# Optimization experiments

Hardware: AMD Instinct MI355X
Metric: run time of the kernel (lower is better)

Reference implementation:

```python
import jax, jax.numpy as jnp
import numpy as np

N, E, CIN, H, OUT, L = 100000, 1200000, 3, 64, 3, 3
EPS = 1e-7  # GENConv message epsilon


def setup_inputs() -> dict:
    key = jax.random.key(0)
    ks = jax.random.split(key, 8)
    f = lambda k, s, sc=0.1: (jax.random.normal(k, s, jnp.float32) * sc)
    return {
        "x": f(ks[0], (N, CIN), 1.0),
        "edge_index": jax.random.randint(ks[1], (2, E), 0, N, jnp.int32),
        "enc_W": f(ks[2], (CIN, H)),
        "enc_b": jnp.zeros((H,), jnp.float32),
        "t": jnp.ones((L,), jnp.float32),
        "mlp_W1": f(ks[3], (L, H, 2 * H)),
        "mlp_b1": jnp.zeros((L, 2 * H), jnp.float32),
        "mlp_g": jnp.ones((L, 2 * H), jnp.float32),
        "mlp_beta": jnp.zeros((L, 2 * H), jnp.float32),
        "mlp_W2": f(ks[4], (L, 2 * H, H)),
        "mlp_b2": jnp.zeros((L, H), jnp.float32),
        "ln_g": jnp.ones((L, H), jnp.float32),
        "ln_b": jnp.zeros((L, H), jnp.float32),
        "lin_W": f(ks[5], (H, OUT)),
        "lin_b": jnp.zeros((OUT,), jnp.float32),
    }


def layer_norm(x, g, b, eps=1e-5):
    mu = jnp.mean(x, -1, keepdims=True)
    var = jnp.var(x, -1, keepdims=True)
    return (x - mu) * jax.lax.rsqrt(var + eps) * g + b


def genconv(x, src, dst, t, W1, b1, g, beta, W2, b2):
    # message: relu(x_j) + eps, per edge  [E, H]
    msg = jax.nn.relu(x[src]) + EPS
    # softmax aggregation with temperature t (per-destination, elementwise)
    logits = msg * t
    m = jax.ops.segment_max(logits, dst, num_segments=N)            # [N, H]
    w = jnp.exp(logits - m[dst])                                    # [E, H]
    denom = jax.ops.segment_sum(w, dst, num_segments=N)             # [N, H]
    agg = jax.ops.segment_sum(msg * (w / denom[dst]), dst, num_segments=N)
    # root residual + MLP [H -> 2H -> LN -> ReLU -> H]
    out = agg + x
    h = jax.nn.relu(layer_norm(out @ W1 + b1, g, beta))
    return h @ W2 + b2


def reference(x, edge_index, enc_W, enc_b, t, mlp_W1, mlp_b1, mlp_g, mlp_beta,
              mlp_W2, mlp_b2, ln_g, ln_b, lin_W, lin_b):
    src, dst = edge_index[0], edge_index[1]
    h = x @ enc_W + enc_b
    # layers[0].conv applied directly (DeepGCN 'res+' convention)
    h = genconv(h, src, dst, t[0], mlp_W1[0], mlp_b1[0], mlp_g[0], mlp_beta[0],
                mlp_W2[0], mlp_b2[0])
    for i in range(1, L):
        z = jax.nn.relu(layer_norm(h, ln_g[i], ln_b[i]))
        h = h + genconv(z, src, dst, t[i], mlp_W1[i], mlp_b1[i], mlp_g[i],
                        mlp_beta[i], mlp_W2[i], mlp_b2[i])
    h = jax.nn.relu(layer_norm(h, ln_g[0], ln_b[0]))
    return h @ lin_W + lin_b
```

## Files before the change

### kernel.cpp

```cpp
#include <hip/hip_runtime.h>
#include <hip/hip_bf16.h>
#include <math.h>

#define H 64
#define H2 128
#define EPS_MSG 1e-7f
#define LN_EPS 1e-5f
#define LOG2E 1.4426950408889634f
#define LN2 0.6931471805599453f
#define YSTR 136
#define BSTRIDE 4608
#define OSTRIDE 5376
#define CHUNK 8192

typedef __attribute__((ext_vector_type(8))) short bf16x8;
typedef __attribute__((ext_vector_type(4))) float f32x4;

__device__ __forceinline__ unsigned short f2bf(float f) {
    union { float f; unsigned int i; } x; x.f = f;
    unsigned int r = x.i + 0x7FFF + ((x.i >> 16) & 1);
    return (unsigned short)(r >> 16);
}

__global__ __launch_bounds__(256) void bscat_k(const int* __restrict__ src,
                                               const int* __restrict__ dst,
                                               int* __restrict__ bcnt,
                                               unsigned int* __restrict__ bdata,
                                               int E, int nbuck) {
    __shared__ int h[512], base[512];
    for (int i = threadIdx.x; i < nbuck; i += 256) h[i] = 0;
    __syncthreads();
    int lo = blockIdx.x * CHUNK;
    int hi = lo + CHUNK; if (hi > E) hi = E;
    for (int i = lo + threadIdx.x; i < hi; i += 256)
        atomicAdd(&h[dst[i] >> 8], 1);
    __syncthreads();
    for (int i = threadIdx.x; i < nbuck; i += 256) {
        int c = h[i];
        base[i] = c ? atomicAdd(&bcnt[i], c) : 0;
        h[i] = 0;
    }
    __syncthreads();
    for (int i = lo + threadIdx.x; i < hi; i += 256) {
        int d = dst[i];
        int b = d >> 8;
        int pos = base[b] + atomicAdd(&h[b], 1);
        bdata[(size_t)b * BSTRIDE + pos] = ((unsigned int)src[i] << 8) | (unsigned int)(d & 255);
    }
}

__global__ __launch_bounds__(256) void bsort_k(const unsigned int* __restrict__ bdata,
                                               const int* __restrict__ bcnt,
                                               int2* __restrict__ rowq,
                                               int* __restrict__ srcs_sorted,
                                               int Nn) {
    __shared__ unsigned int stage[BSTRIDE];
    __shared__ int cnt[256], pre[256], ex[256];
    int b = blockIdx.x, tid = threadIdx.x;
    int m = bcnt[b]; if (m > BSTRIDE) m = BSTRIDE;
    size_t lo = (size_t)b * BSTRIDE;
    int oLo = b * OSTRIDE;
    for (int i = tid; i < m; i += 256) stage[i] = bdata[lo + i];
    cnt[tid] = 0;
    __syncthreads();
    for (int i = tid; i < m; i += 256) atomicAdd(&cnt[stage[i] & 255], 1);
    __syncthreads();
    int myc = cnt[tid];
    int pc = (myc + 3) & ~3;
    pre[tid] = pc;
    __syncthreads();
    #pragma unroll
    for (int off = 1; off < 256; off <<= 1) {
        int t = (tid >= off) ? pre[tid - off] : 0;
        __syncthreads();
        pre[tid] += t;
        __syncthreads();
    }
    int pexcl = pre[tid] - pc;
    ex[tid] = pexcl;
    int node = (b << 8) + tid;
    if (node < Nn) rowq[node] = make_int2(oLo + pexcl, pc >> 2);
    else           rowq[node] = make_int2(0, 0);
    for (int p = myc; p < pc; ++p) srcs_sorted[oLo + pexcl + p] = Nn;
    __syncthreads();
    cnt[tid] = 0;
    __syncthreads();
    for (int i = tid; i < m; i += 256) {
        unsigned int v = stage[i];
        int dl = v & 255;
        int p = ex[dl] + atomicAdd(&cnt[dl], 1);
        srcs_sorted[oLo + p] = (int)(v >> 8);
    }
}

__global__ void wprep_k(const float* __restrict__ W1, const float* __restrict__ W2,
                        unsigned short* __restrict__ Wf1, unsigned short* __restrict__ Wf2) {
    int idx = blockIdx.x * 256 + threadIdx.x;
    const int half = 3 * 8192;
    if (idx < half) {
        int layer = idx / 8192, rem = idx - layer * 8192;
        int t = rem >> 9;
        int l = (rem >> 3) & 63;
        int i = rem & 7;
        int h = t >> 3, ct = t & 7;
        int kpos = h * 32 + (l >> 4) * 8 + i;
        int k = (kpos & 3) * 16 + (kpos >> 2);
        int j = ct * 16 + (l & 15);
        Wf1[idx] = f2bf(W1[(size_t)layer * H * H2 + (size_t)k * H2 + j]);
    } else if (idx < 2 * half) {
        int id2 = idx - half;
        int layer = id2 / 8192, rem = id2 - layer * 8192;
        int t = rem >> 9;
        int l = (rem >> 3) & 63;
        int i = rem & 7;
        int kk = t >> 2, ct2 = t & 3;
        int k = kk * 32 + (l >> 4) * 8 + i;
        int j = ct2 * 16 + (l & 15);
        Wf2[id2] = f2bf(W2[(size_t)layer * H2 * H + (size_t)k * H + j]);
    }
}

__global__ void encoder_k(const float* __restrict__ x, const float* __restrict__ W,
                          const float* __restrict__ b,
                          unsigned short* __restrict__ Zself, unsigned short* __restrict__ Zmsg,
                          const float* __restrict__ t, int Nn) {
    int idx = blockIdx.x * blockDim.x + threadIdx.x;
    if (idx >= (Nn + 1) * H) return;
    int n = idx >> 6, c = idx & 63;
    if (n == Nn) { Zmsg[idx] = f2bf(-200.f); return; }
    float acc = b[c];
    #pragma unroll
    for (int k = 0; k < 3; ++k) acc = fmaf(x[n * 3 + k], W[k * H + c], acc);
    int j = (c & 15) * 4 + (c >> 4);
    Zself[(size_t)n * H + j] = f2bf(acc);
    Zmsg[(size_t)n * H + j]  = f2bf(fmaxf(acc, 0.f) * (LOG2E) * t[0]);
}

__global__ __launch_bounds__(256) void gather_k(
    const unsigned short* __restrict__ Zmsg, const unsigned short* __restrict__ Zself,
    unsigned short* __restrict__ Gbf,
    const int2* __restrict__ rowq,
    const int* __restrict__ srcs,
    const float* __restrict__ t, int layer, int Nn)
{
    int wid = threadIdx.x >> 6, lane = threadIdx.x & 63;
    int nA = (blockIdx.x * 4 + wid) * 4;
    if (nA >= Nn) return;
    int slot = lane >> 4;
    int ch4  = lane & 15;
    float scale = (LN2) * __builtin_amdgcn_rcpf(t[layer]);

    int4 rAB = *(const int4*)&rowq[nA];
    int4 rCD = *(const int4*)&rowq[nA + 2];
    int begA = rAB.x, qA = rAB.y, begB = rAB.z, qB = rAB.w;
    int begC = rCD.x, qC = rCD.y, begD = rCD.z, qD = rCD.w;

    int ns = nA + slot; if (ns >= Nn) ns = Nn - 1;
    const unsigned short* selfTab = (layer == 0) ? Zself : Zmsg;
    uint2 sv = *(const uint2*)(selfTab + (size_t)ns * H + ch4 * 4);

    #define LQ(qq, beg, i)                                                     \
        {                                                                      \
            int s = srcs[(beg) + 4 * (i) + slot];                              \
            qq = *(const uint2*)(Zmsg + (size_t)s * H + ch4 * 4);              \
        }

    uint2 a0={0,0},a1={0,0},a2={0,0},a3={0,0};
    uint2 b0={0,0},b1={0,0},b2={0,0},b3={0,0};
    uint2 c0={0,0},c1={0,0},c2={0,0},c3={0,0};
    uint2 e0={0,0},e1={0,0},e2={0,0},e3={0,0};
    if (qA > 0) LQ(a0, begA, 0)
    if (qB > 0) LQ(b0, begB, 0)
    if (qC > 0) LQ(c0, begC, 0)
    if (qD > 0) LQ(e0, begD, 0)
    if (qA > 1) LQ(a1, begA, 1)
    if (qB > 1) LQ(b1, begB, 1)
    if (qC > 1) LQ(c1, begC, 1)
    if (qD > 1) LQ(e1, begD, 1)
    if (qA > 2) LQ(a2, begA, 2)
    if (qB > 2) LQ(b2, begB, 2)
    if (qC > 2) LQ(c2, begC, 2)
    if (qD > 2) LQ(e2, begD, 2)
    if (qA > 3) LQ(a3, begA, 3)
    if (qB > 3) LQ(b3, begB, 3)
    if (qC > 3) LQ(c3, begC, 3)
    if (qD > 3) LQ(e3, begD, 3)

    float dA0=0.f,dA1=0.f,dA2=0.f,dA3=0.f,sA0=0.f,sA1=0.f,sA2=0.f,sA3=0.f;
    float dB0=0.f,dB1=0.f,dB2=0.f,dB3=0.f,sB0=0.f,sB1=0.f,sB2=0.f,sB3=0.f;
    float dC0=0.f,dC1=0.f,dC2=0.f,dC3=0.f,sC0=0.f,sC1=0.f,sC2=0.f,sC3=0.f;
    float dD0=0.f,dD1=0.f,dD2=0.f,dD3=0.f,sD0=0.f,sD1=0.f,sD2=0.f,sD3=0.f;

    #define PROC(qq, dd0,dd1,dd2,dd3, ss0,ss1,ss2,ss3)                         \
        {                                                                      \
            float u0 = __uint_as_float(qq.x << 16);                            \
            float u1 = __uint_as_float(qq.x & 0xffff0000u);                    \
            float u2 = __uint_as_float(qq.y << 16);                            \
            float u3 = __uint_as_float(qq.y & 0xffff0000u);                    \
            float w0 = __builtin_amdgcn_exp2f(u0);                             \
            float w1 = __builtin_amdgcn_exp2f(u1);                             \
            float w2 = __builtin_amdgcn_exp2f(u2);                             \
            float w3 = __builtin_amdgcn_exp2f(u3);                             \
            dd0 += w0; dd1 += w1; dd2 += w2; dd3 += w3;                        \
            ss0 = fmaf(u0, w0, ss0); ss1 = fmaf(u1, w1, ss1);                  \
            ss2 = fmaf(u2, w2, ss2); ss3 = fmaf(u3, w3, ss3);                  \
        }
    #define PROCA(qq) PROC(qq, dA0,dA1,dA2,dA3, sA0,sA1,sA2,sA3)
    #define PROCB(qq) PROC(qq, dB0,dB1,dB2,dB3, sB0,sB1,sB2,sB3)
    #define PROCC(qq) PROC(qq, dC0,dC1,dC2,dC3, sC0,sC1,sC2,sC3)
    #define PROCD(qq) PROC(qq, dD0,dD1,dD2,dD3, sD0,sD1,sD2,sD3)

    if (qA > 0) {
        int i = 0;
        #pragma unroll 1
        for (; i + 4 < qA; i += 4) {
            PROCA(a0) LQ(a0, begA, i + 4)
            PROCA(a1) if (i + 5 < qA) LQ(a1, begA, i + 5)
            PROCA(a2) if (i + 6 < qA) LQ(a2, begA, i + 6)
            PROCA(a3) if (i + 7 < qA) LQ(a3, begA, i + 7)
        }
        PROCA(a0)
        if (i + 1 < qA) PROCA(a1)
        if (i + 2 < qA) PROCA(a2)
        if (i + 3 < qA) PROCA(a3)
    }
    if (qB > 0) {
        int i = 0;
        #pragma unroll 1
        for (; i + 4 < qB; i += 4) {
            PROCB(b0) LQ(b0, begB, i + 4)
            PROCB(b1) if (i + 5 < qB) LQ(b1, begB, i + 5)
            PROCB(b2) if (i + 6 < qB) LQ(b2, begB, i + 6)
            PROCB(b3) if (i + 7 < qB) LQ(b3, begB, i + 7)
        }
        PROCB(b0)
        if (i + 1 < qB) PROCB(b1)
        if (i + 2 < qB) PROCB(b2)
        if (i + 3 < qB) PROCB(b3)
    }
    if (qC > 0) {
        int i = 0;
        #pragma unroll 1
        for (; i + 4 < qC; i += 4) {
            PROCC(c0) LQ(c0, begC, i + 4)
            PROCC(c1) if (i + 5 < qC) LQ(c1, begC, i + 5)
            PROCC(c2) if (i + 6 < qC) LQ(c2, begC, i + 6)
            PROCC(c3) if (i + 7 < qC) LQ(c3, begC, i + 7)
        }
        PROCC(c0)
        if (i + 1 < qC) PROCC(c1)
        if (i + 2 < qC) PROCC(c2)
        if (i + 3 < qC) PROCC(c3)
    }
    if (qD > 0) {
        int i = 0;
        #pragma unroll 1
        for (; i + 4 < qD; i += 4) {
            PROCD(e0) LQ(e0, begD, i + 4)
            PROCD(e1) if (i + 5 < qD) LQ(e1, begD, i + 5)
            PROCD(e2) if (i + 6 < qD) LQ(e2, begD, i + 6)
            PROCD(e3) if (i + 7 < qD) LQ(e3, begD, i + 7)
        }
        PROCD(e0)
        if (i + 1 < qD) PROCD(e1)
        if (i + 2 < qD) PROCD(e2)
        if (i + 3 < qD) PROCD(e3)
    }
    #undef LQ
    #undef PROC
    #undef PROCA
    #undef PROCB
    #undef PROCC
    #undef PROCD

    #pragma unroll
    for (int o = 16; o <= 32; o <<= 1) {
        dA0 += __shfl_xor(dA0, o, 64); dA1 += __shfl_xor(dA1, o, 64);
        dA2 += __shfl_xor(dA2, o, 64); dA3 += __shfl_xor(dA3, o, 64);
        sA0 += __shfl_xor(sA0, o, 64); sA1 += __shfl_xor(sA1, o, 64);
        sA2 += __shfl_xor(sA2, o, 64); sA3 += __shfl_xor(sA3, o, 64);
        dB0 += __shfl_xor(dB0, o, 64); dB1 += __shfl_xor(dB1, o, 64);
        dB2 += __shfl_xor(dB2, o, 64); dB3 += __shfl_xor(dB3, o, 64);
        sB0 += __shfl_xor(sB0, o, 64); sB1 += __shfl_xor(sB1, o, 64);
        sB2 += __shfl_xor(sB2, o, 64); sB3 += __shfl_xor(sB3, o, 64);
        dC0 += __shfl_xor(dC0, o, 64); dC1 += __shfl_xor(dC1, o, 64);
        dC2 += __shfl_xor(dC2, o, 64); dC3 += __shfl_xor(dC3, o, 64);
        sC0 += __shfl_xor(sC0, o, 64); sC1 += __shfl_xor(sC1, o, 64);
        sC2 += __shfl_xor(sC2, o, 64); sC3 += __shfl_xor(sC3, o, 64);
        dD0 += __shfl_xor(dD0, o, 64); dD1 += __shfl_xor(dD1, o, 64);
        dD2 += __shfl_xor(dD2, o, 64); dD3 += __shfl_xor(dD3, o, 64);
        sD0 += __shfl_xor(sD0, o, 64); sD1 += __shfl_xor(sD1, o, 64);
        sD2 += __shfl_xor(sD2, o, 64); sD3 += __shfl_xor(sD3, o, 64);
    }

    #define SEL(vA, vB, vC, vD) ((slot & 2) ? ((slot & 1) ? (vD) : (vC)) : ((slot & 1) ? (vB) : (vA)))
    float ds0 = SEL(dA0, dB0, dC0, dD0), ds1 = SEL(dA1, dB1, dC1, dD1);
    float ds2 = SEL(dA2, dB2, dC2, dD2), ds3 = SEL(dA3, dB3, dC3, dD3);
    float ss0 = SEL(sA0, sB0, sC0, sD0), ss1 = SEL(sA1, sB1, sC1, sD1);
    float ss2 = SEL(sA2, sB2, sC2, sD2), ss3 = SEL(sA3, sB3, sC3, sD3);
    int   qn  = SEL(qA, qB, qC, qD);
    #undef SEL

    float o0 = __uint_as_float(sv.x << 16);
    float o1 = __uint_as_float(sv.x & 0xffff0000u);
    float o2 = __uint_as_float(sv.y << 16);
    float o3 = __uint_as_float(sv.y & 0xffff0000u);
    if (layer != 0) { o0 *= scale; o1 *= scale; o2 *= scale; o3 *= scale; }
    float t0 = fmaf(ss0 * __builtin_amdgcn_rcpf(ds0), scale, EPS_MSG);
    float t1 = fmaf(ss1 * __builtin_amdgcn_rcpf(ds1), scale, EPS_MSG);
    float t2 = fmaf(ss2 * __builtin_amdgcn_rcpf(ds2), scale, EPS_MSG);
    float t3 = fmaf(ss3 * __builtin_amdgcn_rcpf(ds3), scale, EPS_MSG);
    o0 += (qn > 0) ? t0 : 0.f;
    o1 += (qn > 0) ? t1 : 0.f;
    o2 += (qn > 0) ? t2 : 0.f;
    o3 += (qn > 0) ? t3 : 0.f;

    uint2 pv;
    pv.x = (unsigned int)f2bf(o0) | ((unsigned int)f2bf(o1) << 16);
    pv.y = (unsigned int)f2bf(o2) | ((unsigned int)f2bf(o3) << 16);
    if (nA + slot < Nn)
        *(uint2*)(Gbf + (size_t)(nA + slot) * H + ch4 * 4) = pv;
}

__global__ __launch_bounds__(256) void mlp_k(
    const unsigned short* __restrict__ Gbf, float* __restrict__ B,
    const unsigned short* __restrict__ Wf1, const unsigned short* __restrict__ Wf2,
    const float* __restrict__ b1, const float* __restrict__ g,
    const float* __restrict__ beta, const float* __restrict__ b2,
    unsigned short* __restrict__ Zmsg,
    const float* __restrict__ tptr, const float* __restrict__ ln_g,
    const float* __restrict__ ln_b, const float* __restrict__ lin_W,
    const float* __restrict__ lin_b, float* __restrict__ outp,
    int wlayer, int lnidx, int resid, int mode, int Nn)
{
    __shared__ __align__(16) unsigned short yt[4][16 * YSTR];
    int wid = threadIdx.x >> 6, lane = threadIdx.x & 63;
    int gq = lane >> 4, c = lane & 15;
    int n0 = (blockIdx.x * 4 + wid) * 16;

    Wf1 += (size_t)wlayer * 8192; Wf2 += (size_t)wlayer * 8192;
    b1 += wlayer * H2; g += wlayer * H2; beta += wlayer * H2; b2 += wlayer * H;

    int nA = n0 + c; if (nA >= Nn) nA = Nn - 1;
    bf16x8 a0 = *(const bf16x8*)(Gbf + (size_t)nA * H + gq * 8);
    bf16x8 a1 = *(const bf16x8*)(Gbf + (size_t)nA * H + 32 + gq * 8);

    f32x4 acc[8];
    #pragma unroll
    for (int ct = 0; ct < 8; ++ct) {
        f32x4 z = {0.f, 0.f, 0.f, 0.f};
        bf16x8 w0 = *(const bf16x8*)(Wf1 + (size_t)(ct * 64 + lane) * 8);
        bf16x8 w1 = *(const bf16x8*)(Wf1 + (size_t)((8 + ct) * 64 + lane) * 8);
        z = __builtin_amdgcn_mfma_f32_16x16x32_bf16(a0, w0, z, 0, 0, 0);
        z = __builtin_amdgcn_mfma_f32_16x16x32_bf16(a1, w1, z, 0, 0, 0);
        acc[ct] = z;
    }

    float v[8][4];
    #pragma unroll
    for (int ct = 0; ct < 8; ++ct) {
        float bias = b1[ct * 16 + c];
        #pragma unroll
        for (int r = 0; r < 4; ++r) v[ct][r] = acc[ct][r] + bias;
    }
    float mean[4], inv[4];
    #pragma unroll
    for (int r = 0; r < 4; ++r) {
        float s = 0.f;
        #pragma unroll
        for (int ct = 0; ct < 8; ++ct) s += v[ct][r];
        #pragma unroll
        for (int o = 1; o < 16; o <<= 1) s += __shfl_xor(s, o, 64);
        mean[r] = s * (1.f / H2);
    }
    #pragma unroll
    for (int r = 0; r < 4; ++r) {
        float s = 0.f;
        #pragma unroll
        for (int ct = 0; ct < 8; ++ct) { float d = v[ct][r] - mean[r]; s = fmaf(d, d, s); }
        #pragma unroll
        for (int o = 1; o < 16; o <<= 1) s += __shfl_xor(s, o, 64);
        inv[r] = rsqrtf(s * (1.f / H2) + LN_EPS);
    }
    unsigned short* Y = yt[wid];
    #pragma unroll
    for (int ct = 0; ct < 8; ++ct) {
        float gg = g[ct * 16 + c], bb = beta[ct * 16 + c];
        #pragma unroll
        for (int r = 0; r < 4; ++r) {
            float yv = fmaxf(fmaf((v[ct][r] - mean[r]) * inv[r], gg, bb), 0.f);
            Y[(gq * 4 + r) * YSTR + ct * 16 + c] = f2bf(yv);
        }
    }

    f32x4 acc2[4];
    #pragma unroll
    for (int t = 0; t < 4; ++t) acc2[t] = (f32x4){0.f, 0.f, 0.f, 0.f};
    #pragma unroll
    for (int kk = 0; kk < 4; ++kk) {
        bf16x8 af = *(const bf16x8*)(Y + c * YSTR + kk * 32 + gq * 8);
        #pragma unroll
        for (int t = 0; t < 4; ++t) {
            bf16x8 wf = *(const bf16x8*)(Wf2 + (size_t)((kk * 4 + t) * 64 + lane) * 8);
            acc2[t] = __builtin_amdgcn_mfma_f32_16x16x32_bf16(af, wf, acc2[t], 0, 0, 0);
        }
    }

    float b2v[4], gg2[4], bb2[4], lw[4][3];
    const float* g64 = ln_g + lnidx * H;
    const float* be64 = ln_b + lnidx * H;
    #pragma unroll
    for (int tt = 0; tt < 4; ++tt) {
        b2v[tt] = b2[tt * 16 + c];
        gg2[tt] = g64[tt * 16 + c];
        bb2[tt] = be64[tt * 16 + c];
    }
    if (mode == 1) {
        #pragma unroll
        for (int tt = 0; tt < 4; ++tt)
            #pragma unroll
            for (int k = 0; k < 3; ++k) lw[tt][k] = lin_W[(tt * 16 + c) * 3 + k];
    }
    float kmsg = (mode == 0) ? (LOG2E * tptr[lnidx]) : 0.f;

    #pragma unroll
    for (int r = 0; r < 4; ++r) {
        int n = n0 + gq * 4 + r;
        int nc = (n < Nn) ? n : (Nn - 1);
        float hv[4];
        #pragma unroll
        for (int tt = 0; tt < 4; ++tt) hv[tt] = acc2[tt][r] + b2v[tt];
        if (resid) {
            float4 old = *(const float4*)&B[(size_t)nc * H + c * 4];
            hv[0] += old.x; hv[1] += old.y; hv[2] += old.z; hv[3] += old.w;
        }
        float s = hv[0] + hv[1] + hv[2] + hv[3];
        #pragma unroll
        for (int o = 1; o < 16; o <<= 1) s += __shfl_xor(s, o, 64);
        float mu = s * (1.f / H);
        float q = 0.f;
        #pragma unroll
        for (int tt = 0; tt < 4; ++tt) { float d = hv[tt] - mu; q = fmaf(d, d, q); }
        #pragma unroll
        for (int o = 1; o < 16; o <<= 1) q += __shfl_xor(q, o, 64);
        float iv = rsqrtf(q * (1.f / H) + LN_EPS);
        float z[4];
        #pragma unroll
        for (int tt = 0; tt < 4; ++tt)
            z[tt] = fmaxf(fmaf((hv[tt] - mu) * iv, gg2[tt], bb2[tt]), 0.f);

        if (mode == 0) {
            if (n < Nn) {
                float4 hq = {hv[0], hv[1], hv[2], hv[3]};
                *(float4*)&B[(size_t)n * H + c * 4] = hq;
                uint2 zm;
                zm.x = (unsigned int)f2bf(z[0] * kmsg) | ((unsigned int)f2bf(z[1] * kmsg) << 16);
                zm.y = (unsigned int)f2bf(z[2] * kmsg) | ((unsigned int)f2bf(z[3] * kmsg) << 16);
                *(uint2*)&Zmsg[(size_t)n * H + c * 4] = zm;
            }
        } else {
            float p0 = 0.f, p1 = 0.f, p2 = 0.f;
            #pragma unroll
            for (int tt = 0; tt < 4; ++tt) {
                p0 = fmaf(z[tt], lw[tt][0], p0);
                p1 = fmaf(z[tt], lw[tt][1], p1);
                p2 = fmaf(z[tt], lw[tt][2], p2);
            }
            #pragma unroll
            for (int o = 1; o < 16; o <<= 1) {
                p0 += __shfl_xor(p0, o, 64);
                p1 += __shfl_xor(p1, o, 64);
                p2 += __shfl_xor(p2, o, 64);
            }
            if (c == 0 && n < Nn) {
                outp[(size_t)n * 3 + 0] = p0 + lin_b[0];
                outp[(size_t)n * 3 + 1] = p1 + lin_b[1];
                outp[(size_t)n * 3 + 2] = p2 + lin_b[2];
            }
        }
    }
}

extern "C" void kernel_launch(void* const* d_in, const int* in_sizes, int n_in,
                              void* d_out, int out_size, void* d_ws, size_t ws_size,
                              hipStream_t stream) {
    const float* x        = (const float*)d_in[0];
    const int*   eidx     = (const int*)  d_in[1];
    const float* enc_W    = (const float*)d_in[2];
    const float* enc_b    = (const float*)d_in[3];
    const float* t        = (const float*)d_in[4];
    const float* mlp_W1   = (const float*)d_in[5];
    const float* mlp_b1   = (const float*)d_in[6];
    const float* mlp_g    = (const float*)d_in[7];
    const float* mlp_beta = (const float*)d_in[8];
    const float* mlp_W2   = (const float*)d_in[9];
    const float* mlp_b2   = (const float*)d_in[10];
    const float* ln_g     = (const float*)d_in[11];
    const float* ln_b     = (const float*)d_in[12];
    const float* lin_W    = (const float*)d_in[13];
    const float* lin_b    = (const float*)d_in[14];
    float* out = (float*)d_out;

    const int N = in_sizes[0] / 3;
    const int E = in_sizes[1] / 2;
    const int* src = eidx;
    const int* dst = eidx + E;
    const int nbuck = (N + 255) >> 8;

    float* Bm = (float*)d_ws;
    int2* rowq = (int2*)(Bm + (size_t)N * H);
    int* bcnt      = (int*)(rowq + 512 * 256);
    int* srcs_sorted = bcnt + 512;
    unsigned short* Zself = (unsigned short*)(srcs_sorted + 512 * OSTRIDE);
    unsigned short* Zmsg  = Zself + (size_t)N * H;
    unsigned short* Gbf   = Zmsg + (size_t)(N + 1) * H;
    unsigned short* Wf1   = Gbf + (size_t)N * H;
    unsigned short* Wf2   = Wf1 + 3 * 8192;
    unsigned int* bdata = (unsigned int*)Gbf;

    const int eBlocks = (E + CHUNK - 1) / CHUNK;

    hipMemsetAsync(bcnt, 0, 512 * sizeof(int), stream);
    bscat_k<<<eBlocks, 256, 0, stream>>>(src, dst, bcnt, bdata, E, nbuck);
    bsort_k<<<nbuck, 256, 0, stream>>>(bdata, bcnt, rowq, srcs_sorted, N);

    wprep_k<<<192, 256, 0, stream>>>(mlp_W1, mlp_W2, Wf1, Wf2);
    encoder_k<<<((size_t)(N + 1) * H + 255) / 256, 256, 0, stream>>>(x, enc_W, enc_b, Zself, Zmsg, t, N);

    const int gBlocks   = (N + 15) / 16;
    const int mlpBlocks = (N + 63) / 64;

    gather_k<<<gBlocks, 256, 0, stream>>>(Zmsg, Zself, Gbf, rowq, srcs_sorted, t, 0, N);
    mlp_k<<<mlpBlocks, 256, 0, stream>>>(Gbf, Bm, Wf1, Wf2, mlp_b1, mlp_g, mlp_beta, mlp_b2,
                                         Zmsg, t, ln_g, ln_b, lin_W, lin_b, out,
                                         0, 1, 0, 0, N);
    gather_k<<<gBlocks, 256, 0, stream>>>(Zmsg, Zself, Gbf, rowq, srcs_sorted, t, 1, N);
    mlp_k<<<mlpBlocks, 256, 0, stream>>>(Gbf, Bm, Wf1, Wf2, mlp_b1, mlp_g, mlp_beta, mlp_b2,
                                         Zmsg, t, ln_g, ln_b, lin_W, lin_b, out,
                                         1, 2, 1, 0, N);
    gather_k<<<gBlocks, 256, 0, stream>>>(Zmsg, Zself, Gbf, rowq, srcs_sorted, t, 2, N);
    mlp_k<<<mlpBlocks, 256, 0, stream>>>(Gbf, Bm, Wf1, Wf2, mlp_b1, mlp_g, mlp_beta, mlp_b2,
                                         Zmsg, t, ln_g, ln_b, lin_W, lin_b, out,
                                         2, 0, 1, 1, N);
}
```

Before: 351.2 us.

## Pad node groups to common edge count and interleave four-node gather loops

The sort kernel now pads every group of four consecutive destination nodes to the group's maximum padded degree, storing a has-edges flag in the low bit of the row offset and enlarging the per-bucket output stride. The gather kernel then runs one shared loop for all four nodes, interleaving their loads and exp/accumulate work instead of four serial loops. This is meant to raise memory-level parallelism and cut serial dependency and branch overhead in the gather. In exchange, extra padded dummy edges are processed, and writes are clipped at the new stride, which could drop edges if a bucket overflows.

```diff
diff --git a/kernel.cpp b/kernel.cpp
--- a/kernel.cpp
+++ b/kernel.cpp
@@ -10,7 +10,7 @@
 #define LN2 0.6931471805599453f
 #define YSTR 136
 #define BSTRIDE 4608
-#define OSTRIDE 5376
+#define OSTRIDE 6144
 #define CHUNK 8192
 
 typedef __attribute__((ext_vector_type(8))) short bf16x8;
@@ -55,7 +55,7 @@
                                                int* __restrict__ srcs_sorted,
                                                int Nn) {
     __shared__ unsigned int stage[BSTRIDE];
-    __shared__ int cnt[256], pre[256], ex[256];
+    __shared__ int cnt[256], pre[256], ex[256], pc4[256];
     int b = blockIdx.x, tid = threadIdx.x;
     int m = bcnt[b]; if (m > BSTRIDE) m = BSTRIDE;
     size_t lo = (size_t)b * BSTRIDE;
@@ -67,7 +67,11 @@
     __syncthreads();
     int myc = cnt[tid];
     int pc = (myc + 3) & ~3;
-    pre[tid] = pc;
+    pc4[tid] = pc;
+    __syncthreads();
+    int g0 = tid & ~3;
+    int gmax = max(max(pc4[g0], pc4[g0 + 1]), max(pc4[g0 + 2], pc4[g0 + 3]));
+    pre[tid] = gmax;
     __syncthreads();
     #pragma unroll
     for (int off = 1; off < 256; off <<= 1) {
@@ -76,12 +80,15 @@
         pre[tid] += t;
         __syncthreads();
     }
-    int pexcl = pre[tid] - pc;
+    int pexcl = pre[tid] - gmax;
     ex[tid] = pexcl;
     int node = (b << 8) + tid;
-    if (node < Nn) rowq[node] = make_int2(oLo + pexcl, pc >> 2);
-    else           rowq[node] = make_int2(0, 0);
-    for (int p = myc; p < pc; ++p) srcs_sorted[oLo + pexcl + p] = Nn;
+    if (node < Nn)
+        rowq[node] = make_int2((oLo + pexcl) | (myc > 0 ? 1 : 0), gmax >> 2);
+    for (int p = myc; p < gmax; ++p) {
+        int pos = pexcl + p;
+        if (pos < OSTRIDE) srcs_sorted[oLo + pos] = Nn;
+    }
     __syncthreads();
     cnt[tid] = 0;
     __syncthreads();
@@ -89,7 +96,7 @@
         unsigned int v = stage[i];
         int dl = v & 255;
         int p = ex[dl] + atomicAdd(&cnt[dl], 1);
-        srcs_sorted[oLo + p] = (int)(v >> 8);
+        if (p < OSTRIDE) srcs_sorted[oLo + p] = (int)(v >> 8);
     }
 }
 
@@ -152,8 +159,11 @@
 
     int4 rAB = *(const int4*)&rowq[nA];
     int4 rCD = *(const int4*)&rowq[nA + 2];
-    int begA = rAB.x, qA = rAB.y, begB = rAB.z, qB = rAB.w;
-    int begC = rCD.x, qC = rCD.y, begD = rCD.z, qD = rCD.w;
+    int begA = rAB.x & ~3, hasA = rAB.x & 1;
+    int begB = rAB.z & ~3, hasB = rAB.z & 1;
+    int begC = rCD.x & ~3, hasC = rCD.x & 1;
+    int begD = rCD.z & ~3, hasD = rCD.z & 1;
+    int q = rAB.y;
 
     int ns = nA + slot; if (ns >= Nn) ns = Nn - 1;
     const unsigned short* selfTab = (layer == 0) ? Zself : Zmsg;
@@ -169,22 +179,6 @@
     uint2 b0={0,0},b1={0,0},b2={0,0},b3={0,0};
     uint2 c0={0,0},c1={0,0},c2={0,0},c3={0,0};
     uint2 e0={0,0},e1={0,0},e2={0,0},e3={0,0};
-    if (qA > 0) LQ(a0, begA, 0)
-    if (qB > 0) LQ(b0, begB, 0)
-    if (qC > 0) LQ(c0, begC, 0)
-    if (qD > 0) LQ(e0, begD, 0)
-    if (qA > 1) LQ(a1, begA, 1)
-    if (qB > 1) LQ(b1, begB, 1)
-    if (qC > 1) LQ(c1, begC, 1)
-    if (qD > 1) LQ(e1, begD, 1)
-    if (qA > 2) LQ(a2, begA, 2)
-    if (qB > 2) LQ(b2, begB, 2)
-    if (qC > 2) LQ(c2, begC, 2)
-    if (qD > 2) LQ(e2, begD, 2)
-    if (qA > 3) LQ(a3, begA, 3)
-    if (qB > 3) LQ(b3, begB, 3)
-    if (qC > 3) LQ(c3, begC, 3)
-    if (qD > 3) LQ(e3, begD, 3)
 
     float dA0=0.f,dA1=0.f,dA2=0.f,dA3=0.f,sA0=0.f,sA1=0.f,sA2=0.f,sA3=0.f;
     float dB0=0.f,dB1=0.f,dB2=0.f,dB3=0.f,sB0=0.f,sB1=0.f,sB2=0.f,sB3=0.f;
@@ -210,61 +204,37 @@
     #define PROCC(qq) PROC(qq, dC0,dC1,dC2,dC3, sC0,sC1,sC2,sC3)
     #define PROCD(qq) PROC(qq, dD0,dD1,dD2,dD3, sD0,sD1,sD2,sD3)
 
-    if (qA > 0) {
+    if (q > 0) {
+        LQ(a0, begA, 0) LQ(b0, begB, 0) LQ(c0, begC, 0) LQ(e0, begD, 0)
+        if (q > 1) { LQ(a1, begA, 1) LQ(b1, begB, 1) LQ(c1, begC, 1) LQ(e1, begD, 1) }
+        if (q > 2) { LQ(a2, begA, 2) LQ(b2, begB, 2) LQ(c2, begC, 2) LQ(e2, begD, 2) }
+        if (q > 3) { LQ(a3, begA, 3) LQ(b3, begB, 3) LQ(c3, begC, 3) LQ(e3, begD, 3) }
+
         int i = 0;
         #pragma unroll 1
-        for (; i + 4 < qA; i += 4) {
+        for (; i + 4 < q; i += 4) {
             PROCA(a0) LQ(a0, begA, i + 4)
-            PROCA(a1) if (i + 5 < qA) LQ(a1, begA, i + 5)
-            PROCA(a2) if (i + 6 < qA) LQ(a2, begA, i + 6)
-            PROCA(a3) if (i + 7 < qA) LQ(a3, begA, i + 7)
-        }
-        PROCA(a0)
-        if (i + 1 < qA) PROCA(a1)
-        if (i + 2 < qA) PROCA(a2)
-        if (i + 3 < qA) PROCA(a3)
-    }
-    if (qB > 0) {
-        int i = 0;
-        #pragma unroll 1
-        for (; i + 4 < qB; i += 4) {
             PROCB(b0) LQ(b0, begB, i + 4)
-            PROCB(b1) if (i + 5 < qB) LQ(b1, begB, i + 5)
-            PROCB(b2) if (i + 6 < qB) LQ(b2, begB, i + 6)
-            PROCB(b3) if (i + 7 < qB) LQ(b3, begB, i + 7)
-        }
-        PROCB(b0)
-        if (i + 1 < qB) PROCB(b1)
-        if (i + 2 < qB) PROCB(b2)
-        if (i + 3 < qB) PROCB(b3)
-    }
-    if (qC > 0) {
-        int i = 0;
-        #pragma unroll 1
-        for (; i + 4 < qC; i += 4) {
             PROCC(c0) LQ(c0, begC, i + 4)
-            PROCC(c1) if (i + 5 < qC) LQ(c1, begC, i + 5)
-            PROCC(c2) if (i + 6 < qC) LQ(c2, begC, i + 6)
-            PROCC(c3) if (i + 7 < qC) LQ(c3, begC, i + 7)
-        }
-        PROCC(c0)
-        if (i + 1 < qC) PROCC(c1)
-        if (i + 2 < qC) PROCC(c2)
-        if (i + 3 < qC) PROCC(c3)
-    }
-    if (qD > 0) {
-        int i = 0;
-        #pragma unroll 1
-        for (; i + 4 < qD; i += 4) {
             PROCD(e0) LQ(e0, begD, i + 4)
-            PROCD(e1) if (i + 5 < qD) LQ(e1, begD, i + 5)
-            PROCD(e2) if (i + 6 < qD) LQ(e2, begD, i + 6)
-            PROCD(e3) if (i + 7 < qD) LQ(e3, begD, i + 7)
-        }
-        PROCD(e0)
-        if (i + 1 < qD) PROCD(e1)
-        if (i + 2 < qD) PROCD(e2)
-        if (i + 3 < qD) PROCD(e3)
+            bool c5 = (i + 5 < q), c6 = (i + 6 < q), c7 = (i + 7 < q);
+            PROCA(a1) if (c5) LQ(a1, begA, i + 5)
+            PROCB(b1) if (c5) LQ(b1, begB, i + 5)
+            PROCC(c1) if (c5) LQ(c1, begC, i + 5)
+            PROCD(e1) if (c5) LQ(e1, begD, i + 5)
+            PROCA(a2) if (c6) LQ(a2, begA, i + 6)
+            PROCB(b2) if (c6) LQ(b2, begB, i + 6)
+            PROCC(c2) if (c6) LQ(c2, begC, i + 6)
+            PROCD(e2) if (c6) LQ(e2, begD, i + 6)
+            PROCA(a3) if (c7) LQ(a3, begA, i + 7)
+            PROCB(b3) if (c7) LQ(b3, begB, i + 7)
+            PROCC(c3) if (c7) LQ(c3, begC, i + 7)
+            PROCD(e3) if (c7) LQ(e3, begD, i + 7)
+        }
+        PROCA(a0) PROCB(b0) PROCC(c0) PROCD(e0)
+        if (i + 1 < q) { PROCA(a1) PROCB(b1) PROCC(c1) PROCD(e1) }
+        if (i + 2 < q) { PROCA(a2) PROCB(b2) PROCC(c2) PROCD(e2) }
+        if (i + 3 < q) { PROCA(a3) PROCB(b3) PROCC(c3) PROCD(e3) }
     }
     #undef LQ
     #undef PROC
@@ -298,7 +268,7 @@
     float ds2 = SEL(dA2, dB2, dC2, dD2), ds3 = SEL(dA3, dB3, dC3, dD3);
     float ss0 = SEL(sA0, sB0, sC0, sD0), ss1 = SEL(sA1, sB1, sC1, sD1);
     float ss2 = SEL(sA2, sB2, sC2, sD2), ss3 = SEL(sA3, sB3, sC3, sD3);
-    int   qn  = SEL(qA, qB, qC, qD);
+    int   hn  = SEL(hasA, hasB, hasC, hasD);
     #undef SEL
 
     float o0 = __uint_as_float(sv.x << 16);
@@ -310,10 +280,10 @@
     float t1 = fmaf(ss1 * __builtin_amdgcn_rcpf(ds1), scale, EPS_MSG);
     float t2 = fmaf(ss2 * __builtin_amdgcn_rcpf(ds2), scale, EPS_MSG);
     float t3 = fmaf(ss3 * __builtin_amdgcn_rcpf(ds3), scale, EPS_MSG);
-    o0 += (qn > 0) ? t0 : 0.f;
-    o1 += (qn > 0) ? t1 : 0.f;
-    o2 += (qn > 0) ? t2 : 0.f;
-    o3 += (qn > 0) ? t3 : 0.f;
+    o0 += hn ? t0 : 0.f;
+    o1 += hn ? t1 : 0.f;
+    o2 += hn ? t2 : 0.f;
+    o3 += hn ? t3 : 0.f;
 
     uint2 pv;
     pv.x = (unsigned int)f2bf(o0) | ((unsigned int)f2bf(o1) << 16);
```

Result: faster. 339.3 us (-3.4%).
